# Performance work log

Hardware: AMD Instinct MI355X
Metric: run time of the kernel (lower is better)

## Reference

```python
import jax, jax.numpy as jnp
import numpy as np

N_NODES = 50000
N_EDGES = 600000
D_IN = 128
D_OUT = 128


def setup_inputs() -> dict:
    key = jax.random.key(0)
    k1, k2, k3, k4, k5 = jax.random.split(key, 5)
    feature = jax.random.normal(k1, (N_NODES, D_IN), dtype=jnp.float32)
    W = jax.random.normal(k2, (D_IN, D_OUT), dtype=jnp.float32) * 0.05
    b = jax.random.normal(k3, (D_OUT,), dtype=jnp.float32) * 0.05
    src = jax.random.randint(k4, (N_EDGES,), 0, N_NODES, dtype=jnp.int32)
    dst = jax.random.randint(k5, (N_EDGES,), 0, N_NODES, dtype=jnp.int32)
    return {"feature": feature, "W": W, "b": b, "src": src, "dst": dst}


def reference(feature, W, b, src, dst):
    n = feature.shape[0]
    # message: copy source node feature along each edge  [E, D]
    msgs = feature[src]
    # reduce: mean over incoming messages per destination node
    agg = jax.ops.segment_sum(msgs, dst, num_segments=n)  # [N, D]
    deg = jax.ops.segment_sum(jnp.ones((src.shape[0],), feature.dtype), dst,
                              num_segments=n)  # [N]
    safe_deg = jnp.maximum(deg, 1.0)
    mean_h = agg / safe_deg[:, None]
    # DGL semantics: nodes with no incoming messages keep their original h
    h = jnp.where(deg[:, None] > 0, mean_h, feature)
    # apply: ReLU(W h + b)
    return jax.nn.relu(h @ W + b)
```

## Files before the change

kernel.cpp:

```cpp
#include <hip/hip_runtime.h>

#define D 128

typedef float f32x4 __attribute__((ext_vector_type(4)));
typedef float f32x8 __attribute__((ext_vector_type(8)));
typedef short s16x8 __attribute__((ext_vector_type(8)));
typedef unsigned short u16x8 __attribute__((ext_vector_type(8)));

static __device__ __forceinline__ unsigned short f2bf(float f) {
    unsigned int u = __float_as_uint(f);
    unsigned int r = (u + 0x7FFFu + ((u >> 16) & 1u)) >> 16;
    return (unsigned short)r;
}
static __device__ __forceinline__ float bf2f(unsigned int lo16) {
    return __uint_as_float(lo16 << 16);
}


__global__ void k_prep_rank(const int* __restrict__ dst, int* __restrict__ cnt,
                            int* __restrict__ rank,
                            const float* __restrict__ feature,
                            unsigned short* __restrict__ fb, int E, int NF4,
                            const float* __restrict__ W,
                            unsigned short* __restrict__ wt) {
    int tid = blockIdx.x * blockDim.x + threadIdx.x;
    int stride = gridDim.x * blockDim.x;
    for (int base = tid * 4; base < E; base += stride * 4) {
        if (base + 4 <= E) {
            int4 d4 = *reinterpret_cast<const int4*>(dst + base);
            int4 r4;
            r4.x = atomicAdd(&cnt[d4.x], 1);
            r4.y = atomicAdd(&cnt[d4.y], 1);
            r4.z = atomicAdd(&cnt[d4.z], 1);
            r4.w = atomicAdd(&cnt[d4.w], 1);
            *reinterpret_cast<int4*>(rank + base) = r4;
        } else {
            for (int i = base; i < E; ++i) rank[i] = atomicAdd(&cnt[dst[i]], 1);
        }
    }
    const f32x4* f4 = reinterpret_cast<const f32x4*>(feature);
    ushort4* fb4 = reinterpret_cast<ushort4*>(fb);
    for (int i = tid; i < NF4; i += stride) {
        f32x4 v = f4[i];
        ushort4 o;
        o.x = f2bf(v[0]);
        o.y = f2bf(v[1]);
        o.z = f2bf(v[2]);
        o.w = f2bf(v[3]);
        fb4[i] = o;
    }
    for (int i = tid; i < D * D; i += stride) {
        int n = i >> 7, k = i & 127;
        wt[i] = f2bf(W[k * D + n]);
    }
}

__global__ void k_alloc(const int* __restrict__ cnt, int* __restrict__ offset,
                        int* __restrict__ gtot, int N) {
    int i = blockIdx.x * blockDim.x + threadIdx.x;
    int lane = threadIdx.x & 63;
    int c = (i < N) ? cnt[i] : 0;
    int s = c;
    #pragma unroll
    for (int o = 1; o < 64; o <<= 1) {
        int t = __shfl_up(s, o);
        if (lane >= o) s += t;
    }
    int wavesum = __shfl(s, 63);
    int base = 0;
    if (lane == 0) base = atomicAdd(gtot, wavesum);
    base = __shfl(base, 0);
    if (i < N) offset[i] = base + s - c;
}

__global__ void k_fill_rank(const int* __restrict__ src,
                            const int* __restrict__ dst,
                            const int* __restrict__ rank,
                            const int* __restrict__ offset,
                            unsigned short* __restrict__ srcs, int E) {
    int t = blockIdx.x * blockDim.x + threadIdx.x;
    int base = t * 4;
    if (base >= E) return;
    if (base + 4 <= E) {
        int4 d4 = *reinterpret_cast<const int4*>(dst + base);
        int4 s4 = *reinterpret_cast<const int4*>(src + base);
        int4 r4 = *reinterpret_cast<const int4*>(rank + base);
        int o0 = offset[d4.x];
        int o1 = offset[d4.y];
        int o2 = offset[d4.z];
        int o3 = offset[d4.w];
        srcs[o0 + r4.x] = (unsigned short)s4.x;
        srcs[o1 + r4.y] = (unsigned short)s4.y;
        srcs[o2 + r4.z] = (unsigned short)s4.z;
        srcs[o3 + r4.w] = (unsigned short)s4.w;
    } else {
        for (int i = base; i < E; ++i)
            srcs[offset[dst[i]] + rank[i]] = (unsigned short)src[i];
    }
}

__global__ __launch_bounds__(256) void k_aggregate_u16(
    const unsigned short* __restrict__ fb,
    const unsigned short* __restrict__ srcs, const int* __restrict__ offset,
    const int* __restrict__ cnt, unsigned short* __restrict__ hb, int N) {
    int w = (blockIdx.x * blockDim.x + threadIdx.x) >> 6;
    int lane = threadIdx.x & 63;
    if (w >= N) return;
    int sub = lane >> 4;
    int l15 = lane & 15;
    int n = cnt[w];
    if (n == 0) {
        if (sub == 0) {
            u16x8 v = *reinterpret_cast<const u16x8*>(fb + (size_t)w * D + l15 * 8);
            *reinterpret_cast<u16x8*>(hb + (size_t)w * D + l15 * 8) = v;
        }
        return;
    }
    int base = offset[w];
    f32x8 acc = {0.f, 0.f, 0.f, 0.f, 0.f, 0.f, 0.f, 0.f};
    int j = 0;
    for (; j + 8 <= n; j += 8) {
        int s0 = srcs[base + j + sub];
        int s1 = srcs[base + j + 4 + sub];
        u16x8 v0 = *reinterpret_cast<const u16x8*>(fb + (size_t)s0 * D + l15 * 8);
        u16x8 v1 = *reinterpret_cast<const u16x8*>(fb + (size_t)s1 * D + l15 * 8);
        #pragma unroll
        for (int q = 0; q < 8; ++q) acc[q] += bf2f((unsigned int)(unsigned short)v0[q]);
        #pragma unroll
        for (int q = 0; q < 8; ++q) acc[q] += bf2f((unsigned int)(unsigned short)v1[q]);
    }
    for (; j < n; j += 4) {
        if (j + sub < n) {
            int s0 = srcs[base + j + sub];
            u16x8 v0 = *reinterpret_cast<const u16x8*>(fb + (size_t)s0 * D + l15 * 8);
            #pragma unroll
            for (int q = 0; q < 8; ++q) acc[q] += bf2f((unsigned int)(unsigned short)v0[q]);
        }
    }
    #pragma unroll
    for (int q = 0; q < 8; ++q) acc[q] += __shfl_xor(acc[q], 16);
    #pragma unroll
    for (int q = 0; q < 8; ++q) acc[q] += __shfl_xor(acc[q], 32);
    if (sub == 0) {
        float r = 1.f / (float)n;
        u16x8 o;
        #pragma unroll
        for (int q = 0; q < 8; ++q) o[q] = f2bf(acc[q] * r);
        *reinterpret_cast<u16x8*>(hb + (size_t)w * D + l15 * 8) = o;
    }
}

__global__ __launch_bounds__(256) void k_finalize_mfma(
    const unsigned short* __restrict__ hb, const unsigned short* __restrict__ Wt,
    const float* __restrict__ b, float* __restrict__ out, int N) {
    __shared__ char lds[65536];

    int t = threadIdx.x;
    int row0 = blockIdx.x * 128;

    #pragma unroll
    for (int i = 0; i < 8; ++i) {
        int chunk = i * 256 + t;
        int row = chunk >> 4;
        int c16 = chunk & 15;
        int ldsoff = row * 256 + ((c16 * 16) ^ ((row & 7) << 4));
        f32x4 v = {0.f, 0.f, 0.f, 0.f};
        int grow = row0 + row;
        if (grow < N)
            v = *reinterpret_cast<const f32x4*>(hb + (size_t)grow * D + c16 * 8);
        *reinterpret_cast<f32x4*>(&lds[ldsoff]) = v;
    }
    #pragma unroll
    for (int i = 0; i < 8; ++i) {
        int chunk = i * 256 + t;
        int row = chunk >> 4;
        int c16 = chunk & 15;
        int ldsoff = 32768 + row * 256 + ((c16 * 16) ^ ((row & 7) << 4));
        f32x4 v = *reinterpret_cast<const f32x4*>(Wt + (size_t)row * D + c16 * 8);
        *reinterpret_cast<f32x4*>(&lds[ldsoff]) = v;
    }
    __syncthreads();

    int wv = t >> 6;
    int l = t & 63;
    int l15 = l & 15;
    int lhi = l >> 4;

    f32x4 acc[2][8];
    #pragma unroll
    for (int m = 0; m < 2; ++m)
        #pragma unroll
        for (int n = 0; n < 8; ++n) acc[m][n] = (f32x4){0.f, 0.f, 0.f, 0.f};

    #pragma unroll
    for (int kk = 0; kk < 4; ++kk) {
        int kb = kk * 64 + lhi * 16;
        s16x8 af[2], bf[8];
        #pragma unroll
        for (int m = 0; m < 2; ++m) {
            int r = wv * 32 + m * 16 + l15;
            af[m] = *reinterpret_cast<const s16x8*>(
                &lds[r * 256 + (kb ^ ((r & 7) << 4))]);
        }
        #pragma unroll
        for (int n = 0; n < 8; ++n) {
            int r = n * 16 + l15;
            bf[n] = *reinterpret_cast<const s16x8*>(
                &lds[32768 + r * 256 + (kb ^ ((r & 7) << 4))]);
        }
        #pragma unroll
        for (int m = 0; m < 2; ++m)
            #pragma unroll
            for (int n = 0; n < 8; ++n)
                acc[m][n] = __builtin_amdgcn_mfma_f32_16x16x32_bf16(
                    af[m], bf[n], acc[m][n], 0, 0, 0);
    }

    #pragma unroll
    for (int n = 0; n < 8; ++n) {
        int col = n * 16 + l15;
        float bv = b[col];
        #pragma unroll
        for (int m = 0; m < 2; ++m) {
            int rbase = row0 + wv * 32 + m * 16 + lhi * 4;
            #pragma unroll
            for (int j = 0; j < 4; ++j) {
                int row = rbase + j;
                if (row < N)
                    out[(size_t)row * D + col] = fmaxf(acc[m][n][j] + bv, 0.f);
            }
        }
    }
}

__global__ void k_prep4(const int* __restrict__ dst, int* __restrict__ cnt,
                        const float* __restrict__ feature,
                        unsigned short* __restrict__ fb, int E, int NF4,
                        const float* __restrict__ W,
                        unsigned short* __restrict__ wt) {
    int tid = blockIdx.x * blockDim.x + threadIdx.x;
    int stride = gridDim.x * blockDim.x;
    for (int base = tid * 4; base < E; base += stride * 4) {
        if (base + 4 <= E) {
            int4 d4 = *reinterpret_cast<const int4*>(dst + base);
            atomicAdd(&cnt[d4.x], 1);
            atomicAdd(&cnt[d4.y], 1);
            atomicAdd(&cnt[d4.z], 1);
            atomicAdd(&cnt[d4.w], 1);
        } else {
            for (int i = base; i < E; ++i) atomicAdd(&cnt[dst[i]], 1);
        }
    }
    const f32x4* f4 = reinterpret_cast<const f32x4*>(feature);
    ushort4* fb4 = reinterpret_cast<ushort4*>(fb);
    for (int i = tid; i < NF4; i += stride) {
        f32x4 v = f4[i];
        ushort4 o;
        o.x = f2bf(v[0]);
        o.y = f2bf(v[1]);
        o.z = f2bf(v[2]);
        o.w = f2bf(v[3]);
        fb4[i] = o;
    }
    for (int i = tid; i < D * D; i += stride) {
        int n = i >> 7, k = i & 127;
        wt[i] = f2bf(W[k * D + n]);
    }
}

__global__ void k_alloc2(const int* __restrict__ cnt, int* __restrict__ offset,
                         int* __restrict__ cursor, int* __restrict__ gtot,
                         int N) {
    int i = blockIdx.x * blockDim.x + threadIdx.x;
    int lane = threadIdx.x & 63;
    int c = (i < N) ? cnt[i] : 0;
    int s = c;
    #pragma unroll
    for (int o = 1; o < 64; o <<= 1) {
        int t = __shfl_up(s, o);
        if (lane >= o) s += t;
    }
    int wavesum = __shfl(s, 63);
    int base = 0;
    if (lane == 0) base = atomicAdd(gtot, wavesum);
    base = __shfl(base, 0);
    if (i < N) {
        int off = base + s - c;
        offset[i] = off;
        cursor[i] = off;
    }
}

__global__ void k_fill_u16(const int* __restrict__ src,
                           const int* __restrict__ dst,
                           int* __restrict__ cursor,
                           unsigned short* __restrict__ srcs, int E) {
    int t = blockIdx.x * blockDim.x + threadIdx.x;
    int base = t * 4;
    if (base >= E) return;
    if (base + 4 <= E) {
        int4 d4 = *reinterpret_cast<const int4*>(dst + base);
        int4 s4 = *reinterpret_cast<const int4*>(src + base);
        int p0 = atomicAdd(&cursor[d4.x], 1);
        int p1 = atomicAdd(&cursor[d4.y], 1);
        int p2 = atomicAdd(&cursor[d4.z], 1);
        int p3 = atomicAdd(&cursor[d4.w], 1);
        srcs[p0] = (unsigned short)s4.x;
        srcs[p1] = (unsigned short)s4.y;
        srcs[p2] = (unsigned short)s4.z;
        srcs[p3] = (unsigned short)s4.w;
    } else {
        for (int i = base; i < E; ++i) {
            int p = atomicAdd(&cursor[dst[i]], 1);
            srcs[p] = (unsigned short)src[i];
        }
    }
}

__global__ void gcn_scatter(const float* __restrict__ feature,
                            const int* __restrict__ src,
                            const int* __restrict__ dst,
                            float* __restrict__ agg,
                            float* __restrict__ deg, int n_edges) {
    int gid = blockIdx.x * blockDim.x + threadIdx.x;
    int e = gid >> 6;
    int lane = gid & 63;
    if (e >= n_edges) return;
    int s = src[e];
    int d = dst[e];
    const float2 v =
        *reinterpret_cast<const float2*>(feature + (size_t)s * D + lane * 2);
    float* o = agg + (size_t)d * D + lane * 2;
    atomicAdd(o, v.x);
    atomicAdd(o + 1, v.y);
    if (lane == 0) atomicAdd(deg + d, 1.0f);
}

__global__ __launch_bounds__(256, 2) void gcn_finalize(
    float* __restrict__ inout, const float* __restrict__ feature,
    const float* __restrict__ W, const float* __restrict__ b,
    const float* __restrict__ deg, int n_nodes) {
    __shared__ float Ws[D * D];
    __shared__ float bs[D];
    __shared__ float hs[4][4][D];

    for (int i = threadIdx.x; i < (D * D) / 4; i += blockDim.x)
        reinterpret_cast<float4*>(Ws)[i] = reinterpret_cast<const float4*>(W)[i];
    if (threadIdx.x < D) bs[threadIdx.x] = b[threadIdx.x];
    __syncthreads();

    int wave = threadIdx.x >> 6;
    int lane = threadIdx.x & 63;
    int gwave = (blockIdx.x * blockDim.x + threadIdx.x) >> 6;
    int nwaves = (gridDim.x * blockDim.x) >> 6;
    int ngroups = (n_nodes + 3) / 4;

    for (int g = gwave; g < ngroups; g += nwaves) {
        int row0 = g * 4;
        #pragma unroll
        for (int r = 0; r < 4; ++r) {
            int row = row0 + r;
            if (row < n_nodes) {
                float2 h2;
                float dg = deg[row];
                if (dg > 0.f) {
                    float2 a = *reinterpret_cast<const float2*>(
                        inout + (size_t)row * D + lane * 2);
                    float rd = 1.f / dg;
                    h2.x = a.x * rd;
                    h2.y = a.y * rd;
                } else {
                    h2 = *reinterpret_cast<const float2*>(
                        feature + (size_t)row * D + lane * 2);
                }
                reinterpret_cast<float2*>(hs[wave][r])[lane] = h2;
            }
        }
        float acc2[4][2];
        #pragma unroll
        for (int r = 0; r < 4; ++r) {
            acc2[r][0] = bs[lane];
            acc2[r][1] = bs[lane + 64];
        }
        #pragma unroll 4
        for (int k = 0; k < D; ++k) {
            float w0 = Ws[k * D + lane];
            float w1 = Ws[k * D + lane + 64];
            #pragma unroll
            for (int r = 0; r < 4; ++r) {
                float hk = hs[wave][r][k];
                acc2[r][0] = fmaf(hk, w0, acc2[r][0]);
                acc2[r][1] = fmaf(hk, w1, acc2[r][1]);
            }
        }
        #pragma unroll
        for (int r = 0; r < 4; ++r) {
            int row = row0 + r;
            if (row < n_nodes) {
                inout[(size_t)row * D + lane] = fmaxf(acc2[r][0], 0.f);
                inout[(size_t)row * D + lane + 64] = fmaxf(acc2[r][1], 0.f);
            }
        }
    }
}

extern "C" void kernel_launch(void* const* d_in, const int* in_sizes, int n_in,
                              void* d_out, int out_size, void* d_ws,
                              size_t ws_size, hipStream_t stream) {
    const float* feature = (const float*)d_in[0];
    const float* W = (const float*)d_in[1];
    const float* b = (const float*)d_in[2];
    const int* src = (const int*)d_in[3];
    const int* dst = (const int*)d_in[4];
    int n_edges = in_sizes[3];
    int n_nodes = in_sizes[0] / D;

    float* out = (float*)d_out;
    int block = 256;
    int nrows_pad = ((n_nodes + 127) / 128) * 128;

    size_t intsA = (size_t)2 * n_nodes + 1 + n_edges;
    size_t a_srcs_off = (intsA * sizeof(int) + 255) & ~(size_t)255;
    size_t a_fb_off = (a_srcs_off + (size_t)n_edges * 2 + 255) & ~(size_t)255;
    size_t a_hb_off = (a_fb_off + (size_t)n_nodes * D * 2 + 255) & ~(size_t)255;
    size_t a_wt_off = a_hb_off + (size_t)nrows_pad * D * 2;
    size_t need_a = a_wt_off + (size_t)D * D * 2;

    size_t intsB = (size_t)3 * n_nodes + 1;
    size_t b_srcs_off = intsB * sizeof(int);
    size_t b_fb_off = (b_srcs_off + (size_t)n_edges * 2 + 255) & ~(size_t)255;
    size_t b_hb_off = (b_fb_off + (size_t)n_nodes * D * 2 + 255) & ~(size_t)255;
    size_t b_wt_off = b_hb_off + (size_t)nrows_pad * D * 2;
    size_t need_b = b_wt_off + (size_t)D * D * 2;

    if (n_nodes < 65536 && ws_size >= need_a) {
        int* cnt = (int*)d_ws;
        int* gtot = cnt + n_nodes;
        int* offset = gtot + 1;
        int* rank = offset + n_nodes;
        unsigned short* srcs = (unsigned short*)((char*)d_ws + a_srcs_off);
        unsigned short* fb = (unsigned short*)((char*)d_ws + a_fb_off);
        unsigned short* hb = (unsigned short*)((char*)d_ws + a_hb_off);
        unsigned short* wt = (unsigned short*)((char*)d_ws + a_wt_off);

        hipMemsetAsync(cnt, 0, (size_t)(n_nodes + 1) * sizeof(int), stream);
        k_prep_rank<<<2048, block, 0, stream>>>(dst, cnt, rank, feature, fb,
                                                n_edges, n_nodes * D / 4, W, wt);
        k_alloc<<<(n_nodes + block - 1) / block, block, 0, stream>>>(
            cnt, offset, gtot, n_nodes);
        k_fill_rank<<<(n_edges / 4 + block) / block, block, 0, stream>>>(
            src, dst, rank, offset, srcs, n_edges);
        k_aggregate_u16<<<((size_t)n_nodes * 64 + block - 1) / block, block, 0,
                          stream>>>(fb, srcs, offset, cnt, hb, n_nodes);
        k_finalize_mfma<<<(n_nodes + 127) / 128, block, 0, stream>>>(
            hb, wt, b, out, n_nodes);
    } else if (n_nodes < 65536 && ws_size >= need_b) {
        int* cnt = (int*)d_ws;
        int* gtot = cnt + n_nodes;
        int* offset = gtot + 1;
        int* cursor = offset + n_nodes;
        unsigned short* srcs = (unsigned short*)((char*)d_ws + b_srcs_off);
        unsigned short* fb = (unsigned short*)((char*)d_ws + b_fb_off);
        unsigned short* hb = (unsigned short*)((char*)d_ws + b_hb_off);
        unsigned short* wt = (unsigned short*)((char*)d_ws + b_wt_off);

        hipMemsetAsync(cnt, 0, (size_t)(n_nodes + 1) * sizeof(int), stream);
        k_prep4<<<2048, block, 0, stream>>>(dst, cnt, feature, fb, n_edges,
                                            n_nodes * D / 4, W, wt);
        k_alloc2<<<(n_nodes + block - 1) / block, block, 0, stream>>>(
            cnt, offset, cursor, gtot, n_nodes);
        k_fill_u16<<<(n_edges / 4 + block) / block, block, 0, stream>>>(
            src, dst, cursor, srcs, n_edges);
        k_aggregate_u16<<<((size_t)n_nodes * 64 + block - 1) / block, block, 0,
                          stream>>>(fb, srcs, offset, cnt, hb, n_nodes);
        k_finalize_mfma<<<(n_nodes + 127) / 128, block, 0, stream>>>(
            hb, wt, b, out, n_nodes);
    } else {
        float* deg = (float*)d_ws;
        hipMemsetAsync(out, 0, (size_t)out_size * sizeof(float), stream);
        hipMemsetAsync(deg, 0, (size_t)n_nodes * sizeof(float), stream);
        long long total_threads = (long long)n_edges * 64;
        int grid = (int)((total_threads + block - 1) / block);
        gcn_scatter<<<grid, block, 0, stream>>>(feature, src, dst, out, deg,
                                                n_edges);
        gcn_finalize<<<512, block, 0, stream>>>(out, feature, W, b, deg,
                                                n_nodes);
    }
}
```

Baseline: 105.6 us.

## Fuse neighbor aggregation with MFMA linear layer via LDS staging

Merges the per-node mean aggregation kernel and the bf16 MFMA GEMM kernel into one kernel. Each block aggregates 64 nodes (16 per wave) straight into swizzled LDS, then runs the 64x128x128 matmul with bias and ReLU. This removes the intermediate hb buffer's global write and read plus one kernel launch. The fallback path B (atomic-cursor CSR build) is dropped. In exchange, each wave now processes 16 nodes serially, so there is less memory-level parallelism in the gather, and the GEMM tile per block shrinks.

```diff
diff --git a/kernel.cpp b/kernel.cpp
--- a/kernel.cpp
+++ b/kernel.cpp
@@ -99,220 +99,111 @@
     }
 }
 
-__global__ __launch_bounds__(256) void k_aggregate_u16(
+__global__ __launch_bounds__(256) void k_agg_gemm(
     const unsigned short* __restrict__ fb,
     const unsigned short* __restrict__ srcs, const int* __restrict__ offset,
-    const int* __restrict__ cnt, unsigned short* __restrict__ hb, int N) {
-    int w = (blockIdx.x * blockDim.x + threadIdx.x) >> 6;
-    int lane = threadIdx.x & 63;
-    if (w >= N) return;
+    const int* __restrict__ cnt, const unsigned short* __restrict__ Wt,
+    const float* __restrict__ b, float* __restrict__ out, int N) {
+    __shared__ char lds[49152];
+
+    int t = threadIdx.x;
+    int row0 = blockIdx.x * 64;
+    int wv = t >> 6;
+    int lane = t & 63;
     int sub = lane >> 4;
     int l15 = lane & 15;
-    int n = cnt[w];
-    if (n == 0) {
-        if (sub == 0) {
-            u16x8 v = *reinterpret_cast<const u16x8*>(fb + (size_t)w * D + l15 * 8);
-            *reinterpret_cast<u16x8*>(hb + (size_t)w * D + l15 * 8) = v;
-        }
-        return;
-    }
-    int base = offset[w];
-    f32x8 acc = {0.f, 0.f, 0.f, 0.f, 0.f, 0.f, 0.f, 0.f};
-    int j = 0;
-    for (; j + 8 <= n; j += 8) {
-        int s0 = srcs[base + j + sub];
-        int s1 = srcs[base + j + 4 + sub];
-        u16x8 v0 = *reinterpret_cast<const u16x8*>(fb + (size_t)s0 * D + l15 * 8);
-        u16x8 v1 = *reinterpret_cast<const u16x8*>(fb + (size_t)s1 * D + l15 * 8);
-        #pragma unroll
-        for (int q = 0; q < 8; ++q) acc[q] += bf2f((unsigned int)(unsigned short)v0[q]);
-        #pragma unroll
-        for (int q = 0; q < 8; ++q) acc[q] += bf2f((unsigned int)(unsigned short)v1[q]);
-    }
-    for (; j < n; j += 4) {
-        if (j + sub < n) {
-            int s0 = srcs[base + j + sub];
-            u16x8 v0 = *reinterpret_cast<const u16x8*>(fb + (size_t)s0 * D + l15 * 8);
-            #pragma unroll
-            for (int q = 0; q < 8; ++q) acc[q] += bf2f((unsigned int)(unsigned short)v0[q]);
-        }
-    }
-    #pragma unroll
-    for (int q = 0; q < 8; ++q) acc[q] += __shfl_xor(acc[q], 16);
-    #pragma unroll
-    for (int q = 0; q < 8; ++q) acc[q] += __shfl_xor(acc[q], 32);
-    if (sub == 0) {
-        float r = 1.f / (float)n;
-        u16x8 o;
-        #pragma unroll
-        for (int q = 0; q < 8; ++q) o[q] = f2bf(acc[q] * r);
-        *reinterpret_cast<u16x8*>(hb + (size_t)w * D + l15 * 8) = o;
-    }
-}
-
-__global__ __launch_bounds__(256) void k_finalize_mfma(
-    const unsigned short* __restrict__ hb, const unsigned short* __restrict__ Wt,
-    const float* __restrict__ b, float* __restrict__ out, int N) {
-    __shared__ char lds[65536];
-
-    int t = threadIdx.x;
-    int row0 = blockIdx.x * 128;
 
     #pragma unroll
     for (int i = 0; i < 8; ++i) {
         int chunk = i * 256 + t;
         int row = chunk >> 4;
         int c16 = chunk & 15;
-        int ldsoff = row * 256 + ((c16 * 16) ^ ((row & 7) << 4));
-        f32x4 v = {0.f, 0.f, 0.f, 0.f};
-        int grow = row0 + row;
-        if (grow < N)
-            v = *reinterpret_cast<const f32x4*>(hb + (size_t)grow * D + c16 * 8);
-        *reinterpret_cast<f32x4*>(&lds[ldsoff]) = v;
-    }
-    #pragma unroll
-    for (int i = 0; i < 8; ++i) {
-        int chunk = i * 256 + t;
-        int row = chunk >> 4;
-        int c16 = chunk & 15;
-        int ldsoff = 32768 + row * 256 + ((c16 * 16) ^ ((row & 7) << 4));
+        int ldsoff = 16384 + row * 256 + ((c16 * 16) ^ ((row & 7) << 4));
         f32x4 v = *reinterpret_cast<const f32x4*>(Wt + (size_t)row * D + c16 * 8);
         *reinterpret_cast<f32x4*>(&lds[ldsoff]) = v;
     }
+
+    for (int r = 0; r < 16; ++r) {
+        int lr = wv * 16 + r;
+        int node = row0 + lr;
+        int ldsa = lr * 256 + ((l15 * 16) ^ ((lr & 7) << 4));
+        if (node >= N) continue;
+        int n = cnt[node];
+        if (n == 0) {
+            if (sub == 0) {
+                u16x8 v = *reinterpret_cast<const u16x8*>(fb + (size_t)node * D + l15 * 8);
+                *reinterpret_cast<u16x8*>(&lds[ldsa]) = v;
+            }
+            continue;
+        }
+        int base = offset[node];
+        f32x8 acc = {0.f, 0.f, 0.f, 0.f, 0.f, 0.f, 0.f, 0.f};
+        int j = 0;
+        for (; j + 8 <= n; j += 8) {
+            int s0 = srcs[base + j + sub];
+            int s1 = srcs[base + j + 4 + sub];
+            u16x8 v0 = *reinterpret_cast<const u16x8*>(fb + (size_t)s0 * D + l15 * 8);
+            u16x8 v1 = *reinterpret_cast<const u16x8*>(fb + (size_t)s1 * D + l15 * 8);
+            #pragma unroll
+            for (int q = 0; q < 8; ++q) acc[q] += bf2f((unsigned int)(unsigned short)v0[q]);
+            #pragma unroll
+            for (int q = 0; q < 8; ++q) acc[q] += bf2f((unsigned int)(unsigned short)v1[q]);
+        }
+        for (; j < n; j += 4) {
+            if (j + sub < n) {
+                int s0 = srcs[base + j + sub];
+                u16x8 v0 = *reinterpret_cast<const u16x8*>(fb + (size_t)s0 * D + l15 * 8);
+                #pragma unroll
+                for (int q = 0; q < 8; ++q) acc[q] += bf2f((unsigned int)(unsigned short)v0[q]);
+            }
+        }
+        #pragma unroll
+        for (int q = 0; q < 8; ++q) acc[q] += __shfl_xor(acc[q], 16);
+        #pragma unroll
+        for (int q = 0; q < 8; ++q) acc[q] += __shfl_xor(acc[q], 32);
+        if (sub == 0) {
+            float inv = 1.f / (float)n;
+            u16x8 o;
+            #pragma unroll
+            for (int q = 0; q < 8; ++q) o[q] = f2bf(acc[q] * inv);
+            *reinterpret_cast<u16x8*>(&lds[ldsa]) = o;
+        }
+    }
     __syncthreads();
 
-    int wv = t >> 6;
-    int l = t & 63;
-    int l15 = l & 15;
-    int lhi = l >> 4;
-
-    f32x4 acc[2][8];
-    #pragma unroll
-    for (int m = 0; m < 2; ++m)
-        #pragma unroll
-        for (int n = 0; n < 8; ++n) acc[m][n] = (f32x4){0.f, 0.f, 0.f, 0.f};
+    f32x4 acc[8];
+    #pragma unroll
+    for (int n = 0; n < 8; ++n) acc[n] = (f32x4){0.f, 0.f, 0.f, 0.f};
 
     #pragma unroll
     for (int kk = 0; kk < 4; ++kk) {
-        int kb = kk * 64 + lhi * 16;
-        s16x8 af[2], bf[8];
-        #pragma unroll
-        for (int m = 0; m < 2; ++m) {
-            int r = wv * 32 + m * 16 + l15;
-            af[m] = *reinterpret_cast<const s16x8*>(
-                &lds[r * 256 + (kb ^ ((r & 7) << 4))]);
-        }
+        int kb = kk * 64 + sub * 16;
+        int ra = wv * 16 + l15;
+        s16x8 af = *reinterpret_cast<const s16x8*>(
+            &lds[ra * 256 + (kb ^ ((ra & 7) << 4))]);
+        s16x8 bf[8];
         #pragma unroll
         for (int n = 0; n < 8; ++n) {
-            int r = n * 16 + l15;
+            int rb = n * 16 + l15;
             bf[n] = *reinterpret_cast<const s16x8*>(
-                &lds[32768 + r * 256 + (kb ^ ((r & 7) << 4))]);
-        }
-        #pragma unroll
-        for (int m = 0; m < 2; ++m)
-            #pragma unroll
-            for (int n = 0; n < 8; ++n)
-                acc[m][n] = __builtin_amdgcn_mfma_f32_16x16x32_bf16(
-                    af[m], bf[n], acc[m][n], 0, 0, 0);
+                &lds[16384 + rb * 256 + (kb ^ ((rb & 7) << 4))]);
+        }
+        #pragma unroll
+        for (int n = 0; n < 8; ++n)
+            acc[n] = __builtin_amdgcn_mfma_f32_16x16x32_bf16(af, bf[n], acc[n],
+                                                             0, 0, 0);
     }
 
     #pragma unroll
     for (int n = 0; n < 8; ++n) {
         int col = n * 16 + l15;
         float bv = b[col];
-        #pragma unroll
-        for (int m = 0; m < 2; ++m) {
-            int rbase = row0 + wv * 32 + m * 16 + lhi * 4;
-            #pragma unroll
-            for (int j = 0; j < 4; ++j) {
-                int row = rbase + j;
-                if (row < N)
-                    out[(size_t)row * D + col] = fmaxf(acc[m][n][j] + bv, 0.f);
-            }
-        }
-    }
-}
-
-__global__ void k_prep4(const int* __restrict__ dst, int* __restrict__ cnt,
-                        const float* __restrict__ feature,
-                        unsigned short* __restrict__ fb, int E, int NF4,
-                        const float* __restrict__ W,
-                        unsigned short* __restrict__ wt) {
-    int tid = blockIdx.x * blockDim.x + threadIdx.x;
-    int stride = gridDim.x * blockDim.x;
-    for (int base = tid * 4; base < E; base += stride * 4) {
-        if (base + 4 <= E) {
-            int4 d4 = *reinterpret_cast<const int4*>(dst + base);
-            atomicAdd(&cnt[d4.x], 1);
-            atomicAdd(&cnt[d4.y], 1);
-            atomicAdd(&cnt[d4.z], 1);
-            atomicAdd(&cnt[d4.w], 1);
-        } else {
-            for (int i = base; i < E; ++i) atomicAdd(&cnt[dst[i]], 1);
-        }
-    }
-    const f32x4* f4 = reinterpret_cast<const f32x4*>(feature);
-    ushort4* fb4 = reinterpret_cast<ushort4*>(fb);
-    for (int i = tid; i < NF4; i += stride) {
-        f32x4 v = f4[i];
-        ushort4 o;
-        o.x = f2bf(v[0]);
-        o.y = f2bf(v[1]);
-        o.z = f2bf(v[2]);
-        o.w = f2bf(v[3]);
-        fb4[i] = o;
-    }
-    for (int i = tid; i < D * D; i += stride) {
-        int n = i >> 7, k = i & 127;
-        wt[i] = f2bf(W[k * D + n]);
-    }
-}
-
-__global__ void k_alloc2(const int* __restrict__ cnt, int* __restrict__ offset,
-                         int* __restrict__ cursor, int* __restrict__ gtot,
-                         int N) {
-    int i = blockIdx.x * blockDim.x + threadIdx.x;
-    int lane = threadIdx.x & 63;
-    int c = (i < N) ? cnt[i] : 0;
-    int s = c;
-    #pragma unroll
-    for (int o = 1; o < 64; o <<= 1) {
-        int t = __shfl_up(s, o);
-        if (lane >= o) s += t;
-    }
-    int wavesum = __shfl(s, 63);
-    int base = 0;
-    if (lane == 0) base = atomicAdd(gtot, wavesum);
-    base = __shfl(base, 0);
-    if (i < N) {
-        int off = base + s - c;
-        offset[i] = off;
-        cursor[i] = off;
-    }
-}
-
-__global__ void k_fill_u16(const int* __restrict__ src,
-                           const int* __restrict__ dst,
-                           int* __restrict__ cursor,
-                           unsigned short* __restrict__ srcs, int E) {
-    int t = blockIdx.x * blockDim.x + threadIdx.x;
-    int base = t * 4;
-    if (base >= E) return;
-    if (base + 4 <= E) {
-        int4 d4 = *reinterpret_cast<const int4*>(dst + base);
-        int4 s4 = *reinterpret_cast<const int4*>(src + base);
-        int p0 = atomicAdd(&cursor[d4.x], 1);
-        int p1 = atomicAdd(&cursor[d4.y], 1);
-        int p2 = atomicAdd(&cursor[d4.z], 1);
-        int p3 = atomicAdd(&cursor[d4.w], 1);
-        srcs[p0] = (unsigned short)s4.x;
-        srcs[p1] = (unsigned short)s4.y;
-        srcs[p2] = (unsigned short)s4.z;
-        srcs[p3] = (unsigned short)s4.w;
-    } else {
-        for (int i = base; i < E; ++i) {
-            int p = atomicAdd(&cursor[dst[i]], 1);
-            srcs[p] = (unsigned short)src[i];
+        int rbase = row0 + wv * 16 + sub * 4;
+        #pragma unroll
+        for (int j = 0; j < 4; ++j) {
+            int row = rbase + j;
+            if (row < N)
+                out[(size_t)row * D + col] = fmaxf(acc[n][j] + bv, 0.f);
         }
     }
 }
@@ -417,21 +308,12 @@
 
     float* out = (float*)d_out;
     int block = 256;
-    int nrows_pad = ((n_nodes + 127) / 128) * 128;
 
     size_t intsA = (size_t)2 * n_nodes + 1 + n_edges;
     size_t a_srcs_off = (intsA * sizeof(int) + 255) & ~(size_t)255;
     size_t a_fb_off = (a_srcs_off + (size_t)n_edges * 2 + 255) & ~(size_t)255;
-    size_t a_hb_off = (a_fb_off + (size_t)n_nodes * D * 2 + 255) & ~(size_t)255;
-    size_t a_wt_off = a_hb_off + (size_t)nrows_pad * D * 2;
+    size_t a_wt_off = (a_fb_off + (size_t)n_nodes * D * 2 + 255) & ~(size_t)255;
     size_t need_a = a_wt_off + (size_t)D * D * 2;
-
-    size_t intsB = (size_t)3 * n_nodes + 1;
-    size_t b_srcs_off = intsB * sizeof(int);
-    size_t b_fb_off = (b_srcs_off + (size_t)n_edges * 2 + 255) & ~(size_t)255;
-    size_t b_hb_off = (b_fb_off + (size_t)n_nodes * D * 2 + 255) & ~(size_t)255;
-    size_t b_wt_off = b_hb_off + (size_t)nrows_pad * D * 2;
-    size_t need_b = b_wt_off + (size_t)D * D * 2;
 
     if (n_nodes < 65536 && ws_size >= need_a) {
         int* cnt = (int*)d_ws;
@@ -440,7 +322,6 @@
         int* rank = offset + n_nodes;
         unsigned short* srcs = (unsigned short*)((char*)d_ws + a_srcs_off);
         unsigned short* fb = (unsigned short*)((char*)d_ws + a_fb_off);
-        unsigned short* hb = (unsigned short*)((char*)d_ws + a_hb_off);
         unsigned short* wt = (unsigned short*)((char*)d_ws + a_wt_off);
 
         hipMemsetAsync(cnt, 0, (size_t)(n_nodes + 1) * sizeof(int), stream);
@@ -450,31 +331,8 @@
             cnt, offset, gtot, n_nodes);
         k_fill_rank<<<(n_edges / 4 + block) / block, block, 0, stream>>>(
             src, dst, rank, offset, srcs, n_edges);
-        k_aggregate_u16<<<((size_t)n_nodes * 64 + block - 1) / block, block, 0,
-                          stream>>>(fb, srcs, offset, cnt, hb, n_nodes);
-        k_finalize_mfma<<<(n_nodes + 127) / 128, block, 0, stream>>>(
-            hb, wt, b, out, n_nodes);
-    } else if (n_nodes < 65536 && ws_size >= need_b) {
-        int* cnt = (int*)d_ws;
-        int* gtot = cnt + n_nodes;
-        int* offset = gtot + 1;
-        int* cursor = offset + n_nodes;
-        unsigned short* srcs = (unsigned short*)((char*)d_ws + b_srcs_off);
-        unsigned short* fb = (unsigned short*)((char*)d_ws + b_fb_off);
-        unsigned short* hb = (unsigned short*)((char*)d_ws + b_hb_off);
-        unsigned short* wt = (unsigned short*)((char*)d_ws + b_wt_off);
-
-        hipMemsetAsync(cnt, 0, (size_t)(n_nodes + 1) * sizeof(int), stream);
-        k_prep4<<<2048, block, 0, stream>>>(dst, cnt, feature, fb, n_edges,
-                                            n_nodes * D / 4, W, wt);
-        k_alloc2<<<(n_nodes + block - 1) / block, block, 0, stream>>>(
-            cnt, offset, cursor, gtot, n_nodes);
-        k_fill_u16<<<(n_edges / 4 + block) / block, block, 0, stream>>>(
-            src, dst, cursor, srcs, n_edges);
-        k_aggregate_u16<<<((size_t)n_nodes * 64 + block - 1) / block, block, 0,
-                          stream>>>(fb, srcs, offset, cnt, hb, n_nodes);
-        k_finalize_mfma<<<(n_nodes + 127) / 128, block, 0, stream>>>(
-            hb, wt, b, out, n_nodes);
+        k_agg_gemm<<<(n_nodes + 63) / 64, block, 0, stream>>>(
+            fb, srcs, offset, cnt, wt, b, out, n_nodes);
     } else {
         float* deg = (float*)d_ws;
         hipMemsetAsync(out, 0, (size_t)out_size * sizeof(float), stream);
```

Measured after the change: 147.5 us. 39.6% more time.
